# Performance work log

Measured on AMD Instinct MI355X. Metric: run time of the kernel, lower is better.

## Reference

```python
import jax, jax.numpy as jnp
import numpy as np

EMBED = 2048
HEADS = 16
DFF = 4 * EMBED
EPS = 1e-5


def layernorm(x, g, b):
    mu = jnp.mean(x, axis=-1, keepdims=True)
    var = jnp.var(x, axis=-1, keepdims=True)
    return (x - mu) * jax.lax.rsqrt(var + EPS) * g + b


def setup_inputs() -> dict:
    key = jax.random.key(0)
    ks = jax.random.split(key, 16)
    s = 1.0 / np.sqrt(EMBED)
    sf = 1.0 / np.sqrt(DFF)
    return {
        "x": jax.random.normal(ks[0], (2, 2048, EMBED), jnp.float32),
        "Wq": jax.random.normal(ks[1], (EMBED, EMBED), jnp.float32) * s,
        "bq": jnp.zeros((EMBED,), jnp.float32),
        "Wk": jax.random.normal(ks[2], (EMBED, EMBED), jnp.float32) * s,
        "bk": jnp.zeros((EMBED,), jnp.float32),
        "Wv": jax.random.normal(ks[3], (EMBED, EMBED), jnp.float32) * s,
        "bv": jnp.zeros((EMBED,), jnp.float32),
        "Wo": jax.random.normal(ks[4], (EMBED, EMBED), jnp.float32) * s,
        "bo": jnp.zeros((EMBED,), jnp.float32),
        "g1": jnp.ones((EMBED,), jnp.float32),
        "b1": jnp.zeros((EMBED,), jnp.float32),
        "g2": jnp.ones((EMBED,), jnp.float32),
        "b2": jnp.zeros((EMBED,), jnp.float32),
        "W1": jax.random.normal(ks[5], (EMBED, DFF), jnp.float32) * s,
        "bf1": jnp.zeros((DFF,), jnp.float32),
        "W2": jax.random.normal(ks[6], (DFF, EMBED), jnp.float32) * sf,
        "bf2": jnp.zeros((EMBED,), jnp.float32),
    }


def reference(x, Wq, bq, Wk, bk, Wv, bv, Wo, bo, g1, b1, g2, b2, W1, bf1, W2, bf2):
    B, N, C = x.shape
    H = HEADS
    hd = C // H
    # QKV projections -> [B, H, N, hd]
    def split_heads(t):
        return t.reshape(B, N, H, hd).transpose(0, 2, 1, 3)
    q = split_heads(x @ Wq + bq)
    k = split_heads(x @ Wk + bk)
    v = split_heads(x @ Wv + bv)
    # scores [B, H, N, N]
    attn = jnp.einsum('bhqd,bhkd->bhqk', q, k) / np.sqrt(hd)
    attn = jax.nn.softmax(attn, axis=-1)
    out = jnp.einsum('bhqk,bhkd->bhqd', attn, v)
    out = out.transpose(0, 2, 1, 3).reshape(B, N, C)
    out = out @ Wo + bo
    h = layernorm(x + out, g1, b1)
    ff = jax.nn.gelu(h @ W1 + bf1, approximate=False) @ W2 + bf2
    return layernorm(h + ff, g2, b2)
```

## Files before the change

### kernel.cpp

```cpp
#include <hip/hip_runtime.h>
#include <math.h>

#define EMBED 2048
#define DFF   8192
#define TOK   4096
#define SEQ   2048
#define HEADS 16
#define HD    128
#define LDQ   6144

typedef __attribute__((ext_vector_type(8))) short short8;
typedef __attribute__((ext_vector_type(4))) float f32x4;

__device__ __forceinline__ unsigned short f2bf(float f) {
    unsigned int u = __float_as_uint(f);
    return (unsigned short)((u + 0x7FFFu + ((u >> 16) & 1u)) >> 16);
}
__device__ __forceinline__ float bf2f(unsigned short s) {
    return __uint_as_float(((unsigned int)s) << 16);
}
__device__ __forceinline__ float exp2_fast(float x) {
    return __builtin_amdgcn_exp2f(x);
}

__device__ __forceinline__ void async16(const void* g, void* l) {
    __builtin_amdgcn_global_load_lds((const __attribute__((address_space(1))) void*)g,
                                     (__attribute__((address_space(3))) void*)l, 16, 0, 0);
}

__device__ __forceinline__ float gelu_fast(float v) {
    const float y = 1.5957691216057308f * (v + 0.044715f * v * v * v);
    return v / (1.0f + __expf(-y));
}

template<int BM, int MODE>
__global__ __launch_bounds__(512, 2)
void gemm8p(const unsigned short* __restrict__ A, const unsigned short* __restrict__ B,
            const float* __restrict__ bias, const void* __restrict__ resid,
            unsigned short* __restrict__ C, int M, int N, int K, int lda)
{
    constexpr int ASLICE = BM * 32;
    constexpr int BSLICE = 256 * 32;
    constexpr int LA = BM / 128;
    constexpr int MF = BM / 32;
    __shared__ __align__(16) unsigned short sm[4*ASLICE + 4*BSLICE];

    const int t = threadIdx.x;
    const int w = t >> 6, l = t & 63;
    const int quad = l >> 4, m16 = l & 15;
    const int wm = w >> 2, wn = w & 3;
    const long bm = (long)blockIdx.y * BM, bn = (long)blockIdx.x * 256;

    f32x4 acc[MF][4] = {};

    const unsigned short* Ag = A + (size_t)bm*lda;
    const unsigned short* Bg = B + (size_t)bn*K;

    auto stageA = [&](int buf, int ks, int k0) {
#pragma unroll
        for (int p = 0; p < LA; ++p) {
            const int e = p*512 + t;
            const int r = e >> 2, s = e & 3;
            const int gc = k0 + ks*32 + (s ^ ((r >> 1) & 3))*8;
            async16(Ag + (size_t)r*lda + gc,
                    sm + buf*2*ASLICE + ks*ASLICE + (p*512 + w*64)*8);
        }
    };
    auto stageB = [&](int buf, int ks, int k0) {
#pragma unroll
        for (int p = 0; p < 2; ++p) {
            const int e = p*512 + t;
            const int r = e >> 2, s = e & 3;
            const int gc = k0 + ks*32 + (s ^ ((r >> 1) & 3))*8;
            async16(Bg + (size_t)r*K + gc,
                    sm + 4*ASLICE + buf*2*BSLICE + ks*BSLICE + (p*512 + w*64)*8);
        }
    };

    stageA(0, 0, 0); stageB(0, 0, 0);
    stageA(0, 1, 0); stageB(0, 1, 0);

    const int iters = K >> 6;
    for (int it = 0; it < iters; ++it) {
        const int cur = it & 1;
        const bool pre = (it + 1 < iters);
        const int kn = (it + 1) << 6;

#pragma unroll
        for (int kk = 0; kk < 2; ++kk) {
            if (kk == 0 || pre) {
                if constexpr (BM == 256) asm volatile("s_waitcnt vmcnt(4)" ::: "memory");
                else                     asm volatile("s_waitcnt vmcnt(3)" ::: "memory");
            } else {
                asm volatile("s_waitcnt vmcnt(0)" ::: "memory");
            }
            __builtin_amdgcn_s_barrier();
            if (pre) { stageA(cur ^ 1, kk, kn); stageB(cur ^ 1, kk, kn); }

            const unsigned short* Ab = sm + cur*2*ASLICE + kk*ASLICE;
            const unsigned short* Bb = sm + 4*ASLICE + cur*2*BSLICE + kk*BSLICE;
            short8 afr[MF], bfr[4];
#pragma unroll
            for (int m = 0; m < MF; ++m) {
                const int R = wm*(BM/2) + m*16 + m16;
                const int sl = quad ^ ((R >> 1) & 3);
                afr[m] = *(const short8*)(Ab + R*32 + sl*8);
            }
#pragma unroll
            for (int n = 0; n < 4; ++n) {
                const int R = wn*64 + n*16 + m16;
                const int sl = quad ^ ((R >> 1) & 3);
                bfr[n] = *(const short8*)(Bb + R*32 + sl*8);
            }
            __builtin_amdgcn_s_setprio(1);
#pragma unroll
            for (int m = 0; m < MF; ++m)
#pragma unroll
                for (int n = 0; n < 4; ++n)
                    acc[m][n] = __builtin_amdgcn_mfma_f32_16x16x32_bf16(afr[m], bfr[n], acc[m][n], 0, 0, 0);
            __builtin_amdgcn_s_setprio(0);
        }
    }

    __syncthreads();
    asm volatile("" ::: "memory");
    float* Cs = (float*)sm;
    const int ecol = (t & 31) * 8;
    float bias8[8];
#pragma unroll
    for (int i = 0; i < 8; ++i) bias8[i] = bias[bn + ecol + i];

    constexpr int NP = BM / 64;
#pragma unroll
    for (int p = 0; p < NP; ++p) {
        if (p) __syncthreads();
        constexpr int HW = (NP == 4) ? 2 : 1;
        const int pwm = p / HW;
        const int mp = (NP == 4) ? (p & 1)*4 : 0;
        if (wm == pwm) {
#pragma unroll
            for (int mi = 0; mi < 4; ++mi)
#pragma unroll
                for (int n = 0; n < 4; ++n)
#pragma unroll
                    for (int r = 0; r < 4; ++r)
                        Cs[(mi*16 + quad*4 + r)*260 + wn*64 + n*16 + m16] = acc[mp + mi][n][r];
        }
        __syncthreads();
#pragma unroll
        for (int j = 0; j < 4; ++j) {
            const int row = j*16 + (t >> 5);
            float v[8];
            *(f32x4*)&v[0] = *(const f32x4*)&Cs[row*260 + ecol];
            *(f32x4*)&v[4] = *(const f32x4*)&Cs[row*260 + ecol + 4];
            const long gr = bm + p*64 + row;
            const long go = gr*N + bn + ecol;
            short8 rb16;
            if (MODE == 3) rb16 = *(const short8*)((const unsigned short*)resid + go);
            short8 o;
#pragma unroll
            for (int i = 0; i < 8; ++i) {
                float y = v[i] + bias8[i];
                if (MODE == 3) y += bf2f((unsigned short)rb16[i]);
                if (MODE == 2) y = gelu_fast(y);
                o[i] = (short)f2bf(y);
            }
            *(short8*)&C[go] = o;
        }
    }
}

template<int MODE>
__global__ __launch_bounds__(256, 2)
void gemm_bf16(const unsigned short* __restrict__ A, const unsigned short* __restrict__ B,
               const float* __restrict__ bias, const void* __restrict__ resid,
               unsigned short* __restrict__ C, int M, int N, int K, int lda)
{
    __shared__ __align__(16) float smemf[8448];
    unsigned short* As = (unsigned short*)smemf;
    unsigned short* Bs = As + 8192;
    float* Cs = smemf;

    const int t = threadIdx.x;
    const int w = t >> 6, l = t & 63;
    const int quad = l >> 4, m16 = l & 15;
    const long bm = (long)blockIdx.y * 128, bn = (long)blockIdx.x * 128;
    const int wr = (w >> 1)*64, wc = (w & 1)*64;

    f32x4 acc[4][4] = {};

    const int srow = w*16 + (l >> 2);
    const int sslot = l & 3;
    const unsigned short* Ag = A + (size_t)bm*lda;
    const unsigned short* Bg = B + (size_t)bn*K;

#pragma unroll
    for (int u = 0; u < 2; ++u) {
        const int row = u*64 + srow;
        const int c = sslot ^ ((row >> 1) & 3);
        async16(Ag + (size_t)row*lda + c*8, &As[u*2048 + w*512]);
        async16(Bg + (size_t)row*K   + c*8, &Bs[u*2048 + w*512]);
    }

    const int iters = K >> 5;
    for (int it = 0; it < iters; ++it) {
        __syncthreads();
        if (it + 1 < iters) {
            const int k0 = (it + 1) << 5;
            const int bo = ((it + 1) & 1) * 4096;
#pragma unroll
            for (int u = 0; u < 2; ++u) {
                const int row = u*64 + srow;
                const int c = sslot ^ ((row >> 1) & 3);
                async16(Ag + (size_t)row*lda + k0 + c*8, &As[bo + u*2048 + w*512]);
                async16(Bg + (size_t)row*K   + k0 + c*8, &Bs[bo + u*2048 + w*512]);
            }
        }
        const int co = (it & 1) * 4096;
        short8 af[4], bf[4];
#pragma unroll
        for (int s = 0; s < 4; ++s) {
            const int ra = wr + s*16 + m16;
            const int sla = quad ^ ((ra >> 1) & 3);
            af[s] = *(const short8*)&As[co + ra*32 + sla*8];
            const int rb = wc + s*16 + m16;
            const int slb = quad ^ ((rb >> 1) & 3);
            bf[s] = *(const short8*)&Bs[co + rb*32 + slb*8];
        }
#pragma unroll
        for (int ms = 0; ms < 4; ++ms)
#pragma unroll
            for (int ns = 0; ns < 4; ++ns)
                acc[ms][ns] = __builtin_amdgcn_mfma_f32_16x16x32_bf16(af[ms], bf[ns], acc[ms][ns], 0, 0, 0);
    }

    const int ecol = (t & 15) * 8;
    float bias8[8];
#pragma unroll
    for (int i = 0; i < 8; ++i) bias8[i] = bias[bn + ecol + i];

#pragma unroll
    for (int pass = 0; pass < 2; ++pass) {
        __syncthreads();
        if ((w >> 1) == pass) {
#pragma unroll
            for (int ms = 0; ms < 4; ++ms)
#pragma unroll
                for (int ns = 0; ns < 4; ++ns)
#pragma unroll
                    for (int r = 0; r < 4; ++r)
                        Cs[(ms*16 + quad*4 + r)*132 + wc + ns*16 + m16] = acc[ms][ns][r];
        }
        __syncthreads();
#pragma unroll
        for (int j = 0; j < 4; ++j) {
            const int row = j*16 + (t >> 4);
            float v[8];
            *(f32x4*)&v[0] = *(const f32x4*)&Cs[row*132 + ecol];
            *(f32x4*)&v[4] = *(const f32x4*)&Cs[row*132 + ecol + 4];
            const long gr = bm + pass*64 + row;
            const long go = gr*N + bn + ecol;
            float r8[8];
            if (MODE == 1) {
                *(f32x4*)&r8[0] = *(const f32x4*)((const float*)resid + go);
                *(f32x4*)&r8[4] = *(const f32x4*)((const float*)resid + go + 4);
            }
            short8 rb16;
            if (MODE == 3) rb16 = *(const short8*)((const unsigned short*)resid + go);
            short8 o;
#pragma unroll
            for (int i = 0; i < 8; ++i) {
                float y = v[i] + bias8[i];
                if (MODE == 1) y += r8[i];
                if (MODE == 3) y += bf2f((unsigned short)rb16[i]);
                if (MODE == 2) y = gelu_fast(y);
                o[i] = (short)f2bf(y);
            }
            *(short8*)&C[go] = o;
        }
    }
}

__global__ __launch_bounds__(256, 2)
void attn_flash(unsigned short* __restrict__ qkv)
{
    __shared__ unsigned short Ks2[2][64*128];
    __shared__ unsigned short Vt2[2][128*72];
    __shared__ unsigned short Ps[4*16*72];

    const int t = threadIdx.x;
    const int w = t >> 6, l = t & 63;
    const int quad = l >> 4, m16 = l & 15;

    const int dd = blockIdx.x;
    const int bh = (dd & 7)*4 + ((dd >> 3) >> 4);
    const int qt = (dd >> 3) & 15;
    const int b = bh >> 4, h = bh & 15;

    const long rowq = (long)b*SEQ + qt*128;
    const long rowb = (long)b*SEQ;
    const int qc = h*HD;
    const int kc = EMBED + h*HD;
    const int vc = 2*EMBED + h*HD;

    const int rbase = w*4 + (l >> 4);
    const int slot  = l & 15;
    const int vslot = t & 15;
    const int vrp   = t >> 4;

    unsigned short* QsOv = (unsigned short*)Vt2;

    short8 va[2], vb[2];
#pragma unroll
    for (int u = 0; u < 2; ++u) {
        const int rp = u*16 + vrp;
        va[u] = *(const short8*)(qkv + (rowb + 2*rp    )*LDQ + vc + vslot*8);
        vb[u] = *(const short8*)(qkv + (rowb + 2*rp + 1)*LDQ + vc + vslot*8);
    }
#pragma unroll
    for (int u = 0; u < 8; ++u) {
        const int row = u*16 + rbase;
        const int c = slot ^ ((row >> 1) & 7);
        async16(qkv + (rowq + row)*LDQ + qc + c*8, QsOv + u*2048 + w*512);
    }
#pragma unroll
    for (int u = 0; u < 4; ++u) {
        const int row = u*16 + rbase;
        const int c = slot ^ ((row >> 1) & 7);
        async16(qkv + (rowb + row)*LDQ + kc + c*8, &Ks2[0][u*2048 + w*512]);
    }
    __syncthreads();

    short8 af[2][4];
#pragma unroll
    for (int qh = 0; qh < 2; ++qh)
#pragma unroll
        for (int ks = 0; ks < 4; ++ks) {
            const int row = w*32 + qh*16 + m16;
            const int sl = (4*ks + quad) ^ ((row >> 1) & 7);
            af[qh][ks] = *(const short8*)&QsOv[row*128 + sl*8];
        }
    __syncthreads();

#pragma unroll
    for (int u = 0; u < 2; ++u) {
        const int rp = u*16 + vrp;
#pragma unroll
        for (int i = 0; i < 8; ++i) {
            const int dv = vslot*8 + i;
            const int col = (2*rp) ^ (((dv >> 5) & 3) << 3);
            unsigned int pv = (unsigned int)(unsigned short)va[u][i] |
                              ((unsigned int)(unsigned short)vb[u][i] << 16);
            *(unsigned int*)&Vt2[0][dv*72 + col] = pv;
        }
    }
    __syncthreads();

    f32x4 O[2][8] = {};
    float mrun[2][4], lrun[2][4];
#pragma unroll
    for (int qh = 0; qh < 2; ++qh)
#pragma unroll
        for (int r = 0; r < 4; ++r) { mrun[qh][r] = -1e30f; lrun[qh][r] = 0.f; }
    unsigned short* Pw = Ps + w*16*72;
    const float SC = 0.08838834764831845f * 1.4426950408889634f;

    for (int kt = 0; kt < SEQ/64; ++kt) {
        const int cur = kt & 1;
        const bool pre = (kt + 1 < SEQ/64);
        const long rowkv = rowb + (long)(kt + 1)*64;

        if (pre) {
#pragma unroll
            for (int u = 0; u < 2; ++u) {
                const int rp = u*16 + vrp;
                va[u] = *(const short8*)(qkv + (rowkv + 2*rp    )*LDQ + vc + vslot*8);
                vb[u] = *(const short8*)(qkv + (rowkv + 2*rp + 1)*LDQ + vc + vslot*8);
            }
#pragma unroll
            for (int u = 0; u < 4; ++u) {
                const int row = u*16 + rbase;
                const int c = slot ^ ((row >> 1) & 7);
                async16(qkv + (rowkv + row)*LDQ + kc + c*8, &Ks2[cur^1][u*2048 + w*512]);
            }
        }

        f32x4 S[2][4];
#pragma unroll
        for (int ns = 0; ns < 4; ++ns) {
            f32x4 a0 = {0.f,0.f,0.f,0.f}, a1 = {0.f,0.f,0.f,0.f};
            const int row = ns*16 + m16;
            const int swr = (row >> 1) & 7;
#pragma unroll
            for (int ks = 0; ks < 4; ++ks) {
                const int sl = (4*ks + quad) ^ swr;
                const short8 bfr = *(const short8*)&Ks2[cur][row*128 + sl*8];
                a0 = __builtin_amdgcn_mfma_f32_16x16x32_bf16(af[0][ks], bfr, a0, 0, 0, 0);
                a1 = __builtin_amdgcn_mfma_f32_16x16x32_bf16(af[1][ks], bfr, a1, 0, 0, 0);
            }
#pragma unroll
            for (int r = 0; r < 4; ++r) { a0[r] *= SC; a1[r] *= SC; }
            S[0][ns] = a0; S[1][ns] = a1;
        }

#pragma unroll
        for (int qh = 0; qh < 2; ++qh) {
            float al[4], rs4[4];
#pragma unroll
            for (int r = 0; r < 4; ++r) {
                float tm = fmaxf(fmaxf(S[qh][0][r], S[qh][1][r]), fmaxf(S[qh][2][r], S[qh][3][r]));
                tm = fmaxf(tm, __shfl_xor(tm, 1));
                tm = fmaxf(tm, __shfl_xor(tm, 2));
                tm = fmaxf(tm, __shfl_xor(tm, 4));
                tm = fmaxf(tm, __shfl_xor(tm, 8));
                const float mn = fmaxf(mrun[qh][r], tm);
                al[r] = exp2_fast(mrun[qh][r] - mn);
                mrun[qh][r] = mn;
                rs4[r] = 0.f;
            }
#pragma unroll
            for (int ns = 0; ns < 4; ++ns)
#pragma unroll
                for (int r = 0; r < 4; ++r) {
                    const float p = exp2_fast(S[qh][ns][r] - mrun[qh][r]);
                    rs4[r] += p;
                    Pw[(quad*4 + r)*72 + ns*16 + m16] = f2bf(p);
                }
#pragma unroll
            for (int r = 0; r < 4; ++r) {
                rs4[r] += __shfl_xor(rs4[r], 1);
                rs4[r] += __shfl_xor(rs4[r], 2);
                rs4[r] += __shfl_xor(rs4[r], 4);
                rs4[r] += __shfl_xor(rs4[r], 8);
                lrun[qh][r] = lrun[qh][r]*al[r] + rs4[r];
            }
            if (__any((al[0] != 1.f) | (al[1] != 1.f) | (al[2] != 1.f) | (al[3] != 1.f))) {
#pragma unroll
                for (int i = 0; i < 8; ++i)
#pragma unroll
                    for (int r = 0; r < 4; ++r) O[qh][i][r] *= al[r];
            }

            if (qh == 1 && pre) {
#pragma unroll
                for (int u = 0; u < 2; ++u) {
                    const int rp = u*16 + vrp;
#pragma unroll
                    for (int i = 0; i < 8; ++i) {
                        const int dv = vslot*8 + i;
                        const int col = (2*rp) ^ (((dv >> 5) & 3) << 3);
                        unsigned int pv = (unsigned int)(unsigned short)va[u][i] |
                                          ((unsigned int)(unsigned short)vb[u][i] << 16);
                        *(unsigned int*)&Vt2[cur^1][dv*72 + col] = pv;
                    }
                }
            }

#pragma unroll
            for (int ks2 = 0; ks2 < 2; ++ks2) {
                const short8 ap = *(const short8*)&Pw[m16*72 + ks2*32 + quad*8];
#pragma unroll
                for (int ds = 0; ds < 8; ++ds) {
                    const int dv = ds*16 + m16;
                    const int jcol = (ks2*32 + quad*8) ^ (((dv >> 5) & 3) << 3);
                    const short8 bv = *(const short8*)&Vt2[cur][dv*72 + jcol];
                    O[qh][ds] = __builtin_amdgcn_mfma_f32_16x16x32_bf16(ap, bv, O[qh][ds], 0, 0, 0);
                }
            }
        }

        __syncthreads();
    }

    float inv[2][4];
#pragma unroll
    for (int qh = 0; qh < 2; ++qh)
#pragma unroll
        for (int r = 0; r < 4; ++r) inv[qh][r] = 1.0f / lrun[qh][r];
#pragma unroll
    for (int qh = 0; qh < 2; ++qh)
#pragma unroll
        for (int ds = 0; ds < 8; ++ds)
#pragma unroll
            for (int r = 0; r < 4; ++r) {
                const long row = rowq + w*32 + qh*16 + quad*4 + r;
                qkv[row*LDQ + qc + ds*16 + m16] = f2bf(O[qh][ds][r] * inv[qh][r]);
            }
}

template<int OUTF32>
__global__ __launch_bounds__(256)
void ln_bf16(const unsigned short* __restrict__ X, const float* __restrict__ g,
             const float* __restrict__ be, void* __restrict__ Y)
{
    __shared__ float r1[256], r2[256];
    const int t = threadIdx.x;
    const long row = blockIdx.x;
    const unsigned short* x = X + row*EMBED;
    float v[8];
    const short8 xv = *(const short8*)(x + t*8);
    float s = 0.f, s2 = 0.f;
#pragma unroll
    for (int i = 0; i < 8; ++i) {
        v[i] = bf2f((unsigned short)xv[i]);
        s += v[i]; s2 += v[i]*v[i];
    }
    r1[t] = s; r2[t] = s2;
    __syncthreads();
    for (int k = 128; k > 0; k >>= 1) {
        if (t < k) { r1[t] += r1[t+k]; r2[t] += r2[t+k]; }
        __syncthreads();
    }
    const float mu = r1[0] * (1.0f/EMBED);
    const float var = r2[0] * (1.0f/EMBED) - mu*mu;
    const float rstd = rsqrtf(var + 1e-5f);
    if (OUTF32) {
        float* y = (float*)Y + row*EMBED + t*8;
#pragma unroll
        for (int i = 0; i < 8; ++i) y[i] = (v[i]-mu)*rstd*g[t*8+i] + be[t*8+i];
    } else {
        unsigned short* y = (unsigned short*)Y + row*EMBED;
        short8 o;
#pragma unroll
        for (int i = 0; i < 8; ++i) o[i] = (short)f2bf((v[i]-mu)*rstd*g[t*8+i] + be[t*8+i]);
        *(short8*)(y + t*8) = o;
    }
}

__global__ __launch_bounds__(256)
void cvt_transpose(const float* __restrict__ W, unsigned short* __restrict__ Wt, int K, int N)
{
    __shared__ unsigned short T[32][33];
    const int t = threadIdx.x;
    const long n0 = (long)blockIdx.x*32, k0 = (long)blockIdx.y*32;
    {
        const int r = t >> 3, c = (t & 7)*4;
        const float4 vv = *(const float4*)&W[(k0 + r)*N + n0 + c];
        T[r][c+0] = f2bf(vv.x); T[r][c+1] = f2bf(vv.y);
        T[r][c+2] = f2bf(vv.z); T[r][c+3] = f2bf(vv.w);
    }
    __syncthreads();
    const int rn = t >> 3, kk = (t & 7)*4;
    unsigned int p0 = (unsigned int)T[kk+0][rn] | ((unsigned int)T[kk+1][rn] << 16);
    unsigned int p1 = (unsigned int)T[kk+2][rn] | ((unsigned int)T[kk+3][rn] << 16);
    unsigned int* dst = (unsigned int*)&Wt[(n0 + rn)*K + k0 + kk];
    dst[0] = p0; dst[1] = p1;
}

__global__ __launch_bounds__(256)
void cvt_f32_bf16(const float* __restrict__ X, unsigned short* __restrict__ Y, long n)
{
    const long i = ((long)blockIdx.x*256 + threadIdx.x)*8;
    if (i >= n) return;
    const float4 a = *(const float4*)&X[i];
    const float4 b = *(const float4*)&X[i+4];
    short8 o;
    o[0]=(short)f2bf(a.x); o[1]=(short)f2bf(a.y); o[2]=(short)f2bf(a.z); o[3]=(short)f2bf(a.w);
    o[4]=(short)f2bf(b.x); o[5]=(short)f2bf(b.y); o[6]=(short)f2bf(b.z); o[7]=(short)f2bf(b.w);
    *(short8*)&Y[i] = o;
}

__global__ __launch_bounds__(256)
void concat_bias(const float* __restrict__ bq, const float* __restrict__ bk,
                 const float* __restrict__ bv, float* __restrict__ out)
{
    const int i = blockIdx.x*256 + threadIdx.x;
    if (i < 2048) out[i] = bq[i];
    else if (i < 4096) out[i] = bk[i-2048];
    else if (i < 6144) out[i] = bv[i-4096];
}

extern "C" void kernel_launch(void* const* d_in, const int* in_sizes, int n_in,
                              void* d_out, int out_size, void* d_ws, size_t ws_size,
                              hipStream_t stream)
{
    const float* x   = (const float*)d_in[0];
    const float* Wq  = (const float*)d_in[1];
    const float* bq  = (const float*)d_in[2];
    const float* Wk  = (const float*)d_in[3];
    const float* bk  = (const float*)d_in[4];
    const float* Wv  = (const float*)d_in[5];
    const float* bv  = (const float*)d_in[6];
    const float* Wo  = (const float*)d_in[7];
    const float* bo  = (const float*)d_in[8];
    const float* g1  = (const float*)d_in[9];
    const float* b1  = (const float*)d_in[10];
    const float* g2v = (const float*)d_in[11];
    const float* b2v = (const float*)d_in[12];
    const float* W1  = (const float*)d_in[13];
    const float* bf1 = (const float*)d_in[14];
    const float* W2  = (const float*)d_in[15];
    const float* bf2 = (const float*)d_in[16];
    float* out = (float*)d_out;

    char* ws = (char*)d_ws;
    unsigned short* Wqkvt = (unsigned short*)(ws + 0);
    unsigned short* Wot   = (unsigned short*)(ws + 25165824);
    unsigned short* W1t   = (unsigned short*)(ws + 33554432);
    unsigned short* W2t   = (unsigned short*)(ws + 67108864);
    float*          bqkv  = (float*)         (ws + 100663296);
    char* arenaA = ws + 100687872;
    unsigned short* xb   = (unsigned short*)(arenaA);
    unsigned short* qkv  = (unsigned short*)(arenaA + 16777216);
    unsigned short* res1 = (unsigned short*)(arenaA);
    unsigned short* ff   = (unsigned short*)(arenaA);
    unsigned short* hb   = (unsigned short*)(ws + 167796736);
    unsigned short* res2 = (unsigned short*)(ws + 0);

    const dim3 blk(256);
    const dim3 blk8(512);

    cvt_transpose<<<dim3(64,64),  blk, 0, stream>>>(Wq, Wqkvt,             2048, 2048);
    cvt_transpose<<<dim3(64,64),  blk, 0, stream>>>(Wk, Wqkvt + 2048*2048, 2048, 2048);
    cvt_transpose<<<dim3(64,64),  blk, 0, stream>>>(Wv, Wqkvt + 2*2048*2048, 2048, 2048);
    cvt_transpose<<<dim3(64,64),  blk, 0, stream>>>(Wo, Wot, 2048, 2048);
    cvt_transpose<<<dim3(256,64), blk, 0, stream>>>(W1, W1t, 2048, 8192);
    cvt_transpose<<<dim3(64,256), blk, 0, stream>>>(W2, W2t, 8192, 2048);
    concat_bias<<<dim3(24), blk, 0, stream>>>(bq, bk, bv, bqkv);
    cvt_f32_bf16<<<dim3(4096), blk, 0, stream>>>(x, xb, (long)TOK*EMBED);

    gemm8p<128,0><<<dim3(24,32), blk8, 0, stream>>>(xb, Wqkvt, bqkv, nullptr, qkv, TOK, 6144, 2048, 2048);
    attn_flash<<<dim3(512), blk, 0, stream>>>(qkv);
    gemm_bf16<1><<<dim3(16,32), blk, 0, stream>>>(qkv, Wot, bo, x, res1, TOK, 2048, 2048, 6144);
    ln_bf16<0><<<dim3(4096), blk, 0, stream>>>(res1, g1, b1, hb);
    gemm8p<256,2><<<dim3(32,16), blk8, 0, stream>>>(hb, W1t, bf1, nullptr, ff, TOK, 8192, 2048, 2048);
    gemm8p<128,3><<<dim3(8,32), blk8, 0, stream>>>(ff, W2t, bf2, hb, res2, TOK, 2048, 8192, 8192);
    ln_bf16<1><<<dim3(4096), blk, 0, stream>>>(res2, g2v, b2v, out);
}
```

Baseline: 912.7 us.

## Remap gemm8p workgroups across XCDs and route output projection through gemm8p

Adds a workgroup index remap in gemm8p so that consecutive blocks dispatched round-robin across the 8 XCDs cover contiguous tile regions, which should improve L2 reuse of A/B panels. It also removes the separate 128x128 gemm_bf16 kernel and runs the Wo projection (with fp32 residual add, MODE 1) through the larger 512-thread gemm8p tile with a merged epilogue. The risk is lower occupancy or tail imbalance for the smaller 256-block output GEMM, and the remap assumes the grid size is divisible by 8.

Measured after the change: 912.2 us. No clear change (-0.1%).

```diff
diff --git a/kernel.cpp b/kernel.cpp
--- a/kernel.cpp
+++ b/kernel.cpp
@@ -49,7 +49,13 @@
     const int w = t >> 6, l = t & 63;
     const int quad = l >> 4, m16 = l & 15;
     const int wm = w >> 2, wn = w & 3;
-    const long bm = (long)blockIdx.y * BM, bn = (long)blockIdx.x * 256;
+
+    const int nwg = gridDim.x * gridDim.y;
+    const int orig = blockIdx.y * gridDim.x + blockIdx.x;
+    const int lin = (orig & 7) * (nwg >> 3) + (orig >> 3);
+    const int myt = lin % gridDim.y;
+    const int nxt = lin / gridDim.y;
+    const long bm = (long)myt * BM, bn = (long)nxt * 256;
 
     f32x4 acc[MF][4] = {};
 
@@ -154,111 +160,6 @@
             *(f32x4*)&v[0] = *(const f32x4*)&Cs[row*260 + ecol];
             *(f32x4*)&v[4] = *(const f32x4*)&Cs[row*260 + ecol + 4];
             const long gr = bm + p*64 + row;
-            const long go = gr*N + bn + ecol;
-            short8 rb16;
-            if (MODE == 3) rb16 = *(const short8*)((const unsigned short*)resid + go);
-            short8 o;
-#pragma unroll
-            for (int i = 0; i < 8; ++i) {
-                float y = v[i] + bias8[i];
-                if (MODE == 3) y += bf2f((unsigned short)rb16[i]);
-                if (MODE == 2) y = gelu_fast(y);
-                o[i] = (short)f2bf(y);
-            }
-            *(short8*)&C[go] = o;
-        }
-    }
-}
-
-template<int MODE>
-__global__ __launch_bounds__(256, 2)
-void gemm_bf16(const unsigned short* __restrict__ A, const unsigned short* __restrict__ B,
-               const float* __restrict__ bias, const void* __restrict__ resid,
-               unsigned short* __restrict__ C, int M, int N, int K, int lda)
-{
-    __shared__ __align__(16) float smemf[8448];
-    unsigned short* As = (unsigned short*)smemf;
-    unsigned short* Bs = As + 8192;
-    float* Cs = smemf;
-
-    const int t = threadIdx.x;
-    const int w = t >> 6, l = t & 63;
-    const int quad = l >> 4, m16 = l & 15;
-    const long bm = (long)blockIdx.y * 128, bn = (long)blockIdx.x * 128;
-    const int wr = (w >> 1)*64, wc = (w & 1)*64;
-
-    f32x4 acc[4][4] = {};
-
-    const int srow = w*16 + (l >> 2);
-    const int sslot = l & 3;
-    const unsigned short* Ag = A + (size_t)bm*lda;
-    const unsigned short* Bg = B + (size_t)bn*K;
-
-#pragma unroll
-    for (int u = 0; u < 2; ++u) {
-        const int row = u*64 + srow;
-        const int c = sslot ^ ((row >> 1) & 3);
-        async16(Ag + (size_t)row*lda + c*8, &As[u*2048 + w*512]);
-        async16(Bg + (size_t)row*K   + c*8, &Bs[u*2048 + w*512]);
-    }
-
-    const int iters = K >> 5;
-    for (int it = 0; it < iters; ++it) {
-        __syncthreads();
-        if (it + 1 < iters) {
-            const int k0 = (it + 1) << 5;
-            const int bo = ((it + 1) & 1) * 4096;
-#pragma unroll
-            for (int u = 0; u < 2; ++u) {
-                const int row = u*64 + srow;
-                const int c = sslot ^ ((row >> 1) & 3);
-                async16(Ag + (size_t)row*lda + k0 + c*8, &As[bo + u*2048 + w*512]);
-                async16(Bg + (size_t)row*K   + k0 + c*8, &Bs[bo + u*2048 + w*512]);
-            }
-        }
-        const int co = (it & 1) * 4096;
-        short8 af[4], bf[4];
-#pragma unroll
-        for (int s = 0; s < 4; ++s) {
-            const int ra = wr + s*16 + m16;
-            const int sla = quad ^ ((ra >> 1) & 3);
-            af[s] = *(const short8*)&As[co + ra*32 + sla*8];
-            const int rb = wc + s*16 + m16;
-            const int slb = quad ^ ((rb >> 1) & 3);
-            bf[s] = *(const short8*)&Bs[co + rb*32 + slb*8];
-        }
-#pragma unroll
-        for (int ms = 0; ms < 4; ++ms)
-#pragma unroll
-            for (int ns = 0; ns < 4; ++ns)
-                acc[ms][ns] = __builtin_amdgcn_mfma_f32_16x16x32_bf16(af[ms], bf[ns], acc[ms][ns], 0, 0, 0);
-    }
-
-    const int ecol = (t & 15) * 8;
-    float bias8[8];
-#pragma unroll
-    for (int i = 0; i < 8; ++i) bias8[i] = bias[bn + ecol + i];
-
-#pragma unroll
-    for (int pass = 0; pass < 2; ++pass) {
-        __syncthreads();
-        if ((w >> 1) == pass) {
-#pragma unroll
-            for (int ms = 0; ms < 4; ++ms)
-#pragma unroll
-                for (int ns = 0; ns < 4; ++ns)
-#pragma unroll
-                    for (int r = 0; r < 4; ++r)
-                        Cs[(ms*16 + quad*4 + r)*132 + wc + ns*16 + m16] = acc[ms][ns][r];
-        }
-        __syncthreads();
-#pragma unroll
-        for (int j = 0; j < 4; ++j) {
-            const int row = j*16 + (t >> 4);
-            float v[8];
-            *(f32x4*)&v[0] = *(const f32x4*)&Cs[row*132 + ecol];
-            *(f32x4*)&v[4] = *(const f32x4*)&Cs[row*132 + ecol + 4];
-            const long gr = bm + pass*64 + row;
             const long go = gr*N + bn + ecol;
             float r8[8];
             if (MODE == 1) {
@@ -621,7 +522,7 @@
 
     gemm8p<128,0><<<dim3(24,32), blk8, 0, stream>>>(xb, Wqkvt, bqkv, nullptr, qkv, TOK, 6144, 2048, 2048);
     attn_flash<<<dim3(512), blk, 0, stream>>>(qkv);
-    gemm_bf16<1><<<dim3(16,32), blk, 0, stream>>>(qkv, Wot, bo, x, res1, TOK, 2048, 2048, 6144);
+    gemm8p<128,1><<<dim3(8,32), blk8, 0, stream>>>(qkv, Wot, bo, x, res1, TOK, 2048, 2048, 6144);
     ln_bf16<0><<<dim3(4096), blk, 0, stream>>>(res1, g1, b1, hb);
     gemm8p<256,2><<<dim3(32,16), blk8, 0, stream>>>(hb, W1t, bf1, nullptr, ff, TOK, 8192, 2048, 2048);
     gemm8p<128,3><<<dim3(8,32), blk8, 0, stream>>>(ff, W2t, bf2, hb, res2, TOK, 2048, 8192, 8192);
```
